# Kernel tuning notes

Hardware: AMD Instinct MI355X
Metric: run time of the kernel (lower is better)

The kernel has to match this reference:

```python
import jax, jax.numpy as jnp
import numpy as np

T = 1048576      # signal length
K = 3            # number of IMFs
ALPHA = 2000.0   # bandwidth penalty
TAU = 1e-7       # dual ascent step
TOL = 1e-6       # convergence tolerance
N_ITER = 50      # max fixed-point iterations


def _vmd(x, omega_init):
    T_ = x.shape[0]
    t = jnp.arange(1, T_ + 1, dtype=jnp.float32) / T_
    freqs = t - 0.5 - 1.0 / T_                           # [T]
    f_hat = jnp.fft.fftshift(jnp.fft.fft(x))             # [T] complex
    u0 = jnp.zeros((K, T_), dtype=f_hat.dtype)
    lam0 = jnp.zeros((T_,), dtype=f_hat.dtype)

    def step(carry, n):
        u_prev, lam_prev, omega, done = carry
        base = (freqs[None, :] - omega[:, None]) ** 2    # [K,T]
        # mode k's denom also gets (freqs-omega[k-1])^2 and (freqs-omega[k+1])^2
        nbr = jnp.zeros_like(base).at[1:].add(base[:-1]).at[:-1].add(base[1:])
        denom = base + nbr + TAU ** 2
        u_hat = (f_hat[None, :] - lam_prev[None, :] / 2.0) / (1.0 + ALPHA * denom)
        pw = jnp.real(u_hat) ** 2 + jnp.imag(u_hat) ** 2  # |u_hat|^2, [K,T]
        omega_new = jnp.sum(freqs[None, :] * pw, axis=1) / jnp.sum(pw, axis=1)
        lam_new = lam_prev + TAU * (jnp.sum(u_hat, axis=0) - f_hat)
        # convergence check (every 10th iter), mirrors the original break
        u_diff = jnp.sum(jnp.abs(u_hat - u_prev) ** 2) / jnp.sum(jnp.abs(u_prev) ** 2)
        om_diff = jnp.sum(jnp.abs(omega_new - jnp.roll(omega_new, 1))) / K
        conv = (n % 10 == 0) & (u_diff < TOL) & (om_diff < TOL)
        # freeze state once converged (break-iteration's fresh u_hat is kept)
        u_out = jnp.where(done, u_prev, u_hat)
        lam_out = jnp.where(done, lam_prev, lam_new)
        om_out = jnp.where(done, omega, omega_new)
        return (u_out, lam_out, om_out, done | conv), None

    init = (u0, lam0, omega_init.astype(jnp.float32), jnp.array(False))
    (u_hat, _, _, _), _ = jax.lax.scan(jax.checkpoint(step), init, jnp.arange(N_ITER))
    imfs = jnp.real(jnp.fft.ifft(jnp.fft.ifftshift(u_hat, axes=-1), axis=-1))
    return imfs.astype(jnp.float32)                      # [K,T]


def setup_inputs() -> dict:
    key = jax.random.key(0)
    kx, ko = jax.random.split(key)
    x = jax.random.normal(kx, (T,), dtype=jnp.float32)
    omega_init = jax.random.uniform(ko, (K,), dtype=jnp.float32) * 0.5  # init==1
    return {"x": x, "omega_init": omega_init}


def reference(x, omega_init):
    return _vmd(x, omega_init)
```

## Files before the change

kernel.cpp:

```cpp
#include <hip/hip_runtime.h>
#include <math.h>


#define ALPHA_F 2000.0f
#define TAU_F   1e-7f

static __device__ __forceinline__ int lpad2(int i) { return i + (i >> 4); }
static __device__ __forceinline__ int swz(int i)  { return ((i & 7) << 7) | (i >> 3); }
static __device__ __forceinline__ int swzA(int i) { return ((i & 7) << 6) | (i >> 3); }
static __device__ __forceinline__ float frcp(float x) { return __builtin_amdgcn_rcpf(x); }

typedef float v2f __attribute__((ext_vector_type(2)));
static __device__ __forceinline__ v2f sp(float s) { v2f r; r.x = s; r.y = s; return r; }
static __device__ __forceinline__ v2f v2(float a, float b) { v2f r; r.x = a; r.y = b; return r; }
static __device__ __forceinline__ v2f pkfma(v2f a, v2f b, v2f c)
{ return __builtin_elementwise_fma(a, b, c); }

#define PADN2 1088

template<int CTRL>
static __device__ __forceinline__ float dpp_addf(float v)
{
  int r = __builtin_amdgcn_update_dpp(0, __float_as_int(v), CTRL, 0xf, 0xf, true);
  return v + __int_as_float(r);
}
static __device__ __forceinline__ float wave64_sum(float v)
{
  v = dpp_addf<0x111>(v);
  v = dpp_addf<0x112>(v);
  v = dpp_addf<0x114>(v);
  v = dpp_addf<0x118>(v);
  v = dpp_addf<0x142>(v);
  v = dpp_addf<0x143>(v);
  return v;
}
static __device__ __forceinline__ float row16_sum(float v)
{
  v = dpp_addf<0x111>(v);
  v = dpp_addf<0x112>(v);
  v = dpp_addf<0x114>(v);
  v = dpp_addf<0x118>(v);
  return v;
}
static __device__ __forceinline__ float rdlane(float v, int l)
{
  return __int_as_float(__builtin_amdgcn_readlane(__float_as_int(v), l));
}

template<int SIGN>
static __device__ void fft1024c(float2* A, float2* B)
{
  const int u = threadIdx.x;
#pragma unroll
  for (int st = 0; st < 5; ++st) {
    float2 *in  = (st & 1) ? B : A;
    float2 *out = (st & 1) ? A : B;
    const int quarter = 1 << (2 * st);
    const int p = u & (quarter - 1);
    const int g = u >> (2 * st);

    float w1r, w1i;
    if (st == 0) { w1r = 1.0f; w1i = 0.0f; }
    else {
      float sw, cw;
      sincospif((float)(2 * p) * (1.0f / (float)(4 << (2 * st))), &sw, &cw);
      w1r = cw; w1i = (SIGN < 0) ? -sw : sw;
    }
    const float w2r = w1r*w1r - w1i*w1i,  w2i = 2.0f*w1r*w1i;
    const float w3r = w2r*w1r - w2i*w1i,  w3i = w2r*w1i + w2i*w1r;

    float2 X0 = in[lpad2(u      )];
    float2 X1 = in[lpad2(u + 256)];
    float2 X2 = in[lpad2(u + 512)];
    float2 X3 = in[lpad2(u + 768)];

    float y1r = X1.x*w1r - X1.y*w1i, y1i = X1.x*w1i + X1.y*w1r;
    float y2r = X2.x*w2r - X2.y*w2i, y2i = X2.x*w2i + X2.y*w2r;
    float y3r = X3.x*w3r - X3.y*w3i, y3i = X3.x*w3i + X3.y*w3r;

    float t0r = X0.x + y2r, t0i = X0.y + y2i;
    float t1r = X0.x - y2r, t1i = X0.y - y2i;
    float t2r = y1r + y3r,  t2i = y1i + y3i;
    float t3r = y1r - y3r,  t3i = y1i - y3i;

    float o0r = t0r + t2r, o0i = t0i + t2i;
    float o2r = t0r - t2r, o2i = t0i - t2i;
    float o1r, o1i, o3r, o3i;
    if (SIGN < 0) {
      o1r = t1r + t3i; o1i = t1i - t3r;
      o3r = t1r - t3i; o3i = t1i + t3r;
    } else {
      o1r = t1r - t3i; o1i = t1i + t3r;
      o3r = t1r + t3i; o3i = t1i - t3r;
    }
    const int base = (g << (2 * st + 2)) + p;
    out[lpad2(base              )] = make_float2(o0r, o0i);
    out[lpad2(base +     quarter)] = make_float2(o1r, o1i);
    out[lpad2(base + 2 * quarter)] = make_float2(o2r, o2i);
    out[lpad2(base + 3 * quarter)] = make_float2(o3r, o3i);
    __syncthreads();
  }
}

__global__ __launch_bounds__(256) void k_fwd_passA(const float* __restrict__ x,
                                                   float2* __restrict__ ws0)
{
  __shared__ float2 A[PADN2], B[PADN2];
  const int p = swzA(blockIdx.x);
  const int tid = threadIdx.x;
  const int c0 = 2 * p;
#pragma unroll
  for (int q = 0; q < 4; ++q) {
    int j = tid + 256 * q;
    A[lpad2(j)] = ((const float2*)x)[(size_t)j * 512 + p];
  }
  __syncthreads();
  fft1024c<-1>(A, B);
#pragma unroll
  for (int q = 0; q < 4; ++q) {
    int k = tid + 256 * q;
    int kk = (1024 - k) & 1023;
    float2 Z = B[lpad2(k)];
    float2 Wv = B[lpad2(kk)];
    float X0r = 0.5f * (Z.x + Wv.x), X0i = 0.5f * (Z.y - Wv.y);
    float X1r = 0.5f * (Z.y + Wv.y), X1i = 0.5f * (Wv.x - Z.x);
    int ph0 = c0 * k;
    int ph1 = ph0 + k;
    float s0, cc0, s1, cc1;
    sincospif((float)ph0 * (2.0f / 1048576.0f), &s0, &cc0);
    sincospif((float)ph1 * (2.0f / 1048576.0f), &s1, &cc1);
    float4 o;
    o.x = X0r * cc0 + X0i * s0; o.y = X0i * cc0 - X0r * s0;
    o.z = X1r * cc1 + X1i * s1; o.w = X1i * cc1 - X1r * s1;
    ((float4*)ws0)[(size_t)k * 512 + p] = o;
  }
}

__global__ __launch_bounds__(256) void k_fwd_passB(const float2* __restrict__ ws0,
                                                   float2* __restrict__ fhat,
                                                   float* __restrict__ ET)
{
  __shared__ float2 A[PADN2], B[PADN2];
  const int b = swz(blockIdx.x);
  const int tid = threadIdx.x;
#pragma unroll
  for (int q = 0; q < 4; ++q) {
    int j = tid + 256 * q;
    A[lpad2(j)] = ws0[(size_t)b * 1024 + j];
  }
  __syncthreads();
  fft1024c<-1>(A, B);
#pragma unroll
  for (int q = 0; q < 4; ++q) {
    int k2 = tid + 256 * q;
    float2 v = B[lpad2(k2)];
    fhat[(size_t)b * 1024 + k2] = v;
    ET[(size_t)k2 * 1024 + b] = v.x * v.x + v.y * v.y;
  }
}

static __device__ __forceinline__ void lag4(float x, float& l0, float& l1,
                                            float& l2, float& l3)
{
  float m0 = x, m1 = x - (1.0f / 3.0f), m2 = x - (2.0f / 3.0f), m3 = x - 1.0f;
  l0 = -4.5f * m1 * m2 * m3;
  l1 = 13.5f * m0 * m2 * m3;
  l2 = -13.5f * m0 * m1 * m3;
  l3 =  4.5f * m0 * m1 * m2;
}

__global__ __launch_bounds__(256) void k_moments(const float* __restrict__ ET,
                                                 double* __restrict__ W)
{
  __shared__ double red[4 * 4];
  const int B = blockIdx.x;
  const int k2 = B ^ 512;
  const int tid = threadIdx.x;
  double a0 = 0, a1 = 0, a2 = 0, a3 = 0;
#pragma unroll
  for (int q = 0; q < 4; ++q) {
    int k1 = tid + 256 * q;
    float e = ET[(size_t)k2 * 1024 + k1];
    float l0, l1, l2, l3;
    lag4((float)k1 * (1.0f / 1024.0f), l0, l1, l2, l3);
    a0 += (double)(e * l0); a1 += (double)(e * l1);
    a2 += (double)(e * l2); a3 += (double)(e * l3);
  }
  const int lane = tid & 63, wv = tid >> 6;
  double pv[4] = { a0, a1, a2, a3 };
#pragma unroll
  for (int j = 0; j < 4; ++j) {
    double v = pv[j];
    for (int off = 32; off; off >>= 1) v += __shfl_down(v, off, 64);
    if (lane == 0) red[wv * 4 + j] = v;
  }
  __syncthreads();
  if (tid < 4)
    W[B * 4 + tid] = red[tid] + red[4 + tid] + red[8 + tid] + red[12 + tid];
}

__global__ __launch_bounds__(1024) void k_solve(
    const double* __restrict__ W4, const float* __restrict__ omega_init,
    float* __restrict__ ckeepN, float* __restrict__ omegaF)
{
  __shared__ float red[2][6 * 16];
  const int t = threadIdx.x;
  const int lane = t & 63, wv = t >> 6;

  float Wsc[4], fsc[4];
#pragma unroll
  for (int e = 0; e < 4; ++e) {
    Wsc[e] = (float)W4[t * 4 + e];
    fsc[e] = (float)((double)t / 1024.0 + (double)e / 3072.0 - 0.5);
  }
  const v2f frP = v2(fsc[0], fsc[1]), frQ = v2(fsc[2], fsc[3]);
  const v2f WrP = v2(Wsc[0], Wsc[1]), WrQ = v2(Wsc[2], Wsc[3]);
  const v2f WfP = WrP * frP,          WfQ = WrQ * frQ;
  v2f cnrP = sp(0.0f), cnrQ = sp(0.0f);

  float om0 = omega_init[0], om1 = omega_init[1], om2 = omega_init[2];

#pragma unroll 1
  for (int it = 0; it < 49; ++it) {
    float* rb = red[it & 1];
    v2f p0 = sp(0.f), p1 = sp(0.f), p2 = sp(0.f),
        p3 = sp(0.f), p4 = sp(0.f), p5 = sp(0.f);

    auto node_pair = [&](const v2f fv, const v2f Wrv, const v2f Wfv, v2f& cnv) {
      v2f a0 = fv - sp(om0), a1 = fv - sp(om1), a2 = fv - sp(om2);
      v2f d0 = a0 * a0, d1 = a1 * a1, d2 = a2 * a2;
      v2f s01 = d0 + d1, s12 = d1 + d2;
      v2f dA = pkfma(sp(ALPHA_F), s01, sp(1.0f));
      v2f dC = pkfma(sp(ALPHA_F), s12, sp(1.0f));
      v2f dB = pkfma(sp(ALPHA_F), d2, dA);
      v2f AB = dA * dB, BC = dB * dC, AC = dA * dC;
      v2f ABC = AB * dC;
      v2f r = v2(frcp(ABC.x), frcp(ABC.y));
      v2f w0 = BC * r, w1 = AC * r, w2 = AB * r;
      v2f hf = pkfma(sp(-0.5f), cnv, sp(1.0f));
      v2f g = hf * hf;
      v2f gw0 = g * (w0 * w0), gw1 = g * (w1 * w1), gw2 = g * (w2 * w2);
      p0 = pkfma(Wfv, gw0, p0); p1 = pkfma(Wfv, gw1, p1); p2 = pkfma(Wfv, gw2, p2);
      p3 = pkfma(Wrv, gw0, p3); p4 = pkfma(Wrv, gw1, p4); p5 = pkfma(Wrv, gw2, p5);
      v2f S = (w0 + w1) + w2;
      cnv = pkfma(sp(TAU_F), pkfma(S, hf, sp(-1.0f)), cnv);
    };
    node_pair(frP, WrP, WfP, cnrP);
    node_pair(frQ, WrQ, WfQ, cnrQ);

    float q0 = p0.x + p0.y, q1 = p1.x + p1.y, q2 = p2.x + p2.y;
    float q3 = p3.x + p3.y, q4 = p4.x + p4.y, q5 = p5.x + p5.y;

    q0 = wave64_sum(q0); q1 = wave64_sum(q1); q2 = wave64_sum(q2);
    q3 = wave64_sum(q3); q4 = wave64_sum(q4); q5 = wave64_sum(q5);
    if (lane == 63) {
      rb[0 * 16 + wv] = q0; rb[1 * 16 + wv] = q1; rb[2 * 16 + wv] = q2;
      rb[3 * 16 + wv] = q3; rb[4 * 16 + wv] = q4; rb[5 * 16 + wv] = q5;
    }
    __syncthreads();
    float v1 = rb[lane];
    float v2_ = rb[64 + (lane & 31)];
    v1 = row16_sum(v1);
    v2_ = row16_sum(v2_);
    float n0 = rdlane(v1, 15), n1 = rdlane(v1, 31), n2 = rdlane(v1, 47);
    float e0 = rdlane(v1, 63), e1 = rdlane(v2_, 15), e2 = rdlane(v2_, 31);
    om0 = n0 * frcp(e0);
    om1 = n1 * frcp(e1);
    om2 = n2 * frcp(e2);
  }

  ((float4*)ckeepN)[t] = make_float4(cnrP.x, cnrP.y, cnrQ.x, cnrQ.y);
  if (t == 0) { omegaF[0] = om0; omegaF[1] = om1; omegaF[2] = om2; }
}

__global__ __launch_bounds__(256) void k_inv_A2(
    const float2* __restrict__ fhat, const float* __restrict__ ckeepN,
    const float* __restrict__ omegaF, float2* __restrict__ ws0)
{
  __shared__ float2 A[PADN2], B[PADN2];
  __shared__ float cn4[4096];
  __shared__ float som[3];
  const int tid = threadIdx.x;
  const int pk = blockIdx.x >> 10;
  const int b = swz(blockIdx.x & 1023);
  for (int i = tid; i < 4096; i += 256) cn4[i] = ckeepN[i];
  if (tid == 0) { som[0] = omegaF[0]; som[1] = omegaF[1]; som[2] = omegaF[2]; }
  __syncthreads();
  const float om0 = som[0], om1 = som[1], om2 = som[2];
  const float xb = (float)b * (1.0f / 1024.0f);
  float l0, l1, l2, l3, m0, m1, m2, m3;
  lag4(xb, l0, l1, l2, l3);
  lag4(1.0f - xb, m0, m1, m2, m3);

#pragma unroll
  for (int q = 0; q < 4; ++q) {
    int j = tid + 256 * q;
    float2 f = fhat[(size_t)b * 1024 + j];
    int bin = j ^ 512;
    int binp = 1023 - bin;
    float4 cv = ((const float4*)cn4)[bin];
    float4 cw = ((const float4*)cn4)[binp];
    float c  = l0 * cv.x + l1 * cv.y + l2 * cv.z + l3 * cv.w;
    float cp = m0 * cw.x + m1 * cw.y + m2 * cw.z + m3 * cw.w;
    float hf = 1.0f - 0.5f * c;
    float hp = 1.0f - 0.5f * cp;
    int tt = (bin << 10) | b;
    float freq = (float)tt * (1.0f / 1048576.0f) - 0.5f;
    float a0 = freq - om0, a1 = freq - om1, a2 = freq - om2;
    float d0 = a0 * a0, d1 = a1 * a1, d2 = a2 * a2;
    float g0 = -freq - om0, g1 = -freq - om1, g2 = -freq - om2;
    float e0 = g0 * g0, e1 = g1 * g1, e2 = g2 * g2;
    float2 V;
    if (pk == 0) {
      float r0  = hf * frcp(1.0f + ALPHA_F * (d0 + d1));
      float r0n = hp * frcp(1.0f + ALPHA_F * (e0 + e1));
      float r1  = hf * frcp(1.0f + ALPHA_F * (d0 + d1 + d2));
      float r1n = hp * frcp(1.0f + ALPHA_F * (e0 + e1 + e2));
      float Rr = 0.5f * (r0 + r0n);
      float Ri = 0.5f * (r1 + r1n);
      V = make_float2(f.x * Rr - f.y * Ri, f.x * Ri + f.y * Rr);
    } else {
      float r2  = hf * frcp(1.0f + ALPHA_F * (d1 + d2));
      float r2n = hp * frcp(1.0f + ALPHA_F * (e1 + e2));
      float Rr = 0.5f * (r2 + r2n);
      V = make_float2(f.x * Rr, f.y * Rr);
    }
    A[lpad2(j)] = V;
  }
  __syncthreads();
  fft1024c<1>(A, B);
#pragma unroll
  for (int q = 0; q < 4; ++q) {
    int m1i = tid + 256 * q;
    int ph = b * m1i;
    float s, c;
    sincospif((float)ph * (2.0f / 1048576.0f), &s, &c);
    float2 v = B[lpad2(m1i)];
    ws0[(size_t)pk * 1048576 + (size_t)m1i * 1024 + b]
        = make_float2(v.x * c - v.y * s, v.y * c + v.x * s);
  }
}

__global__ __launch_bounds__(256) void k_inv_B2(const float2* __restrict__ ws0,
                                                float* __restrict__ out)
{
  __shared__ float2 A[PADN2], B[PADN2];
  const int pk = blockIdx.x >> 10;
  const int b = swz(blockIdx.x & 1023);
  const int tid = threadIdx.x;
#pragma unroll
  for (int q = 0; q < 4; ++q) {
    int j = tid + 256 * q;
    A[lpad2(j)] = ws0[(size_t)pk * 1048576 + (size_t)b * 1024 + j];
  }
  __syncthreads();
  fft1024c<1>(A, B);
  const float sc = 1.0f / 1048576.0f;
#pragma unroll
  for (int q = 0; q < 4; ++q) {
    int m2 = tid + 256 * q;
    float2 v = B[lpad2(m2)];
    if (pk == 0) {
      out[(size_t)m2 * 1024 + b]           = v.x * sc;
      out[1048576 + (size_t)m2 * 1024 + b] = v.y * sc;
    } else {
      out[2097152 + (size_t)m2 * 1024 + b] = v.x * sc;
    }
  }
}

extern "C" void kernel_launch(void* const* d_in, const int* in_sizes, int n_in,
                              void* d_out, int out_size, void* d_ws, size_t ws_size,
                              hipStream_t stream)
{
  (void)in_sizes; (void)n_in; (void)out_size; (void)ws_size;
  const float* x       = (const float*)d_in[0];
  const float* om_init = (const float*)d_in[1];
  float* out = (float*)d_out;

  char* w = (char*)d_ws;
  const size_t MB = 1024ull * 1024ull;
  float2* fhat     = (float2*)(w);
  float*  ET       = (float*)(w + 8 * MB);
  double* W4       = (double*)(w + 12 * MB);
  float*  ckeepN   = (float*)(w + 12 * MB + 32 * 1024);
  float*  omegaF   = (float*)(w + 12 * MB + 48 * 1024);
  float2* scratch  = (float2*)(w + 16 * MB);

  k_fwd_passA<<<512, 256, 0, stream>>>(x, scratch);
  k_fwd_passB<<<1024, 256, 0, stream>>>(scratch, fhat, ET);
  k_moments<<<1024, 256, 0, stream>>>(ET, W4);
  k_solve<<<1, 1024, 0, stream>>>(W4, om_init, ckeepN, omegaF);
  k_inv_A2<<<2048, 256, 0, stream>>>(fhat, ckeepN, omegaF, scratch);
  k_inv_B2<<<2048, 256, 0, stream>>>(scratch, out);
}
```

Before: 184.0 us.

## Precompute FFT twiddle table, recur post-FFT twiddles, and use packed float2 math

Adds a small kernel that builds radix-4 twiddle tables for both FFT directions once; each FFT block stages the table into LDS instead of calling sincospi per stage. The first radix-4 stage is specialised to drop its trivial twiddles. The inter-pass twiddles in the forward and inverse first passes now come from a complex recurrence instead of two sincospi calls per element. Butterflies and the Wiener filter use packed v2f math. The trade-offs are an extra kernel launch, more LDS per block (which may lower occupancy), and some accuracy loss from the recurrence.

Result: slower. 190.1 us (+3.3%).

```diff
diff --git a/kernel.cpp b/kernel.cpp
--- a/kernel.cpp
+++ b/kernel.cpp
@@ -15,6 +15,12 @@
 static __device__ __forceinline__ v2f v2(float a, float b) { v2f r; r.x = a; r.y = b; return r; }
 static __device__ __forceinline__ v2f pkfma(v2f a, v2f b, v2f c)
 { return __builtin_elementwise_fma(a, b, c); }
+static __device__ __forceinline__ v2f cmul(v2f a, v2f w)
+{
+  v2f t = a * sp(w.x);
+  v2f s = v2(-a.y, a.x);
+  return pkfma(s, sp(w.y), t);
+}
 
 #define PADN2 1088
 
@@ -47,114 +53,148 @@
   return __int_as_float(__builtin_amdgcn_readlane(__float_as_int(v), l));
 }
 
+__global__ __launch_bounds__(256) void k_twid(float2* __restrict__ tw)
+{
+  int i = threadIdx.x + blockIdx.x * 256;
+  if (i >= 340) return;
+  int st, p;
+  if (i < 4)       { st = 1; p = i; }
+  else if (i < 20) { st = 2; p = i - 4; }
+  else if (i < 84) { st = 3; p = i - 20; }
+  else             { st = 4; p = i - 84; }
+  float sw, cw;
+  sincospif((float)(2 * p) * (1.0f / (float)(4 << (2 * st))), &sw, &cw);
+#pragma unroll
+  for (int dir = 0; dir < 2; ++dir) {
+    float w1r = cw, w1i = dir ? sw : -sw;
+    float w2r = w1r * w1r - w1i * w1i, w2i = 2.0f * w1r * w1i;
+    float w3r = w2r * w1r - w2i * w1i, w3i = w2r * w1i + w2i * w1r;
+    float2* b = tw + dir * 1020;
+    b[i]       = make_float2(w1r, w1i);
+    b[340 + i] = make_float2(w2r, w2i);
+    b[680 + i] = make_float2(w3r, w3i);
+  }
+}
+
 template<int SIGN>
-static __device__ void fft1024c(float2* A, float2* B)
+static __device__ void fft1024p(v2f* A, v2f* B, const v2f* __restrict__ twl)
 {
   const int u = threadIdx.x;
-#pragma unroll
-  for (int st = 0; st < 5; ++st) {
-    float2 *in  = (st & 1) ? B : A;
-    float2 *out = (st & 1) ? A : B;
+  {
+    v2f X0 = A[lpad2(u)], X1 = A[lpad2(u + 256)];
+    v2f X2 = A[lpad2(u + 512)], X3 = A[lpad2(u + 768)];
+    v2f t0 = X0 + X2, t1 = X0 - X2, t2 = X1 + X3, t3 = X1 - X3;
+    v2f o0 = t0 + t2, o2 = t0 - t2;
+    v2f s3 = t3.yx;
+    v2f ns3 = v2(s3.x, -s3.y);
+    v2f o1, o3;
+    if (SIGN < 0) { o1 = t1 + ns3; o3 = t1 - ns3; }
+    else          { o1 = t1 - ns3; o3 = t1 + ns3; }
+    const int base = u << 2;
+    B[lpad2(base    )] = o0; B[lpad2(base + 1)] = o1;
+    B[lpad2(base + 2)] = o2; B[lpad2(base + 3)] = o3;
+    __syncthreads();
+  }
+#pragma unroll
+  for (int st = 1; st < 5; ++st) {
+    v2f *in  = (st & 1) ? B : A;
+    v2f *out = (st & 1) ? A : B;
     const int quarter = 1 << (2 * st);
     const int p = u & (quarter - 1);
     const int g = u >> (2 * st);
-
-    float w1r, w1i;
-    if (st == 0) { w1r = 1.0f; w1i = 0.0f; }
-    else {
-      float sw, cw;
-      sincospif((float)(2 * p) * (1.0f / (float)(4 << (2 * st))), &sw, &cw);
-      w1r = cw; w1i = (SIGN < 0) ? -sw : sw;
-    }
-    const float w2r = w1r*w1r - w1i*w1i,  w2i = 2.0f*w1r*w1i;
-    const float w3r = w2r*w1r - w2i*w1i,  w3i = w2r*w1i + w2i*w1r;
-
-    float2 X0 = in[lpad2(u      )];
-    float2 X1 = in[lpad2(u + 256)];
-    float2 X2 = in[lpad2(u + 512)];
-    float2 X3 = in[lpad2(u + 768)];
-
-    float y1r = X1.x*w1r - X1.y*w1i, y1i = X1.x*w1i + X1.y*w1r;
-    float y2r = X2.x*w2r - X2.y*w2i, y2i = X2.x*w2i + X2.y*w2r;
-    float y3r = X3.x*w3r - X3.y*w3i, y3i = X3.x*w3i + X3.y*w3r;
-
-    float t0r = X0.x + y2r, t0i = X0.y + y2i;
-    float t1r = X0.x - y2r, t1i = X0.y - y2i;
-    float t2r = y1r + y3r,  t2i = y1i + y3i;
-    float t3r = y1r - y3r,  t3i = y1i - y3i;
-
-    float o0r = t0r + t2r, o0i = t0i + t2i;
-    float o2r = t0r - t2r, o2i = t0i - t2i;
-    float o1r, o1i, o3r, o3i;
-    if (SIGN < 0) {
-      o1r = t1r + t3i; o1i = t1i - t3r;
-      o3r = t1r - t3i; o3i = t1i + t3r;
-    } else {
-      o1r = t1r - t3i; o1i = t1i + t3r;
-      o3r = t1r + t3i; o3i = t1i - t3r;
-    }
+    const int ti = (quarter - 4) / 3 + p;
+
+    v2f w1 = twl[ti], w2 = twl[340 + ti], w3 = twl[680 + ti];
+
+    v2f X0 = in[lpad2(u)], X1 = in[lpad2(u + 256)];
+    v2f X2 = in[lpad2(u + 512)], X3 = in[lpad2(u + 768)];
+
+    v2f y1 = cmul(X1, w1), y2 = cmul(X2, w2), y3 = cmul(X3, w3);
+
+    v2f t0 = X0 + y2, t1 = X0 - y2, t2 = y1 + y3, t3 = y1 - y3;
+    v2f o0 = t0 + t2, o2 = t0 - t2;
+    v2f s3 = t3.yx;
+    v2f ns3 = v2(s3.x, -s3.y);
+    v2f o1, o3;
+    if (SIGN < 0) { o1 = t1 + ns3; o3 = t1 - ns3; }
+    else          { o1 = t1 - ns3; o3 = t1 + ns3; }
+
     const int base = (g << (2 * st + 2)) + p;
-    out[lpad2(base              )] = make_float2(o0r, o0i);
-    out[lpad2(base +     quarter)] = make_float2(o1r, o1i);
-    out[lpad2(base + 2 * quarter)] = make_float2(o2r, o2i);
-    out[lpad2(base + 3 * quarter)] = make_float2(o3r, o3i);
+    out[lpad2(base              )] = o0;
+    out[lpad2(base +     quarter)] = o1;
+    out[lpad2(base + 2 * quarter)] = o2;
+    out[lpad2(base + 3 * quarter)] = o3;
     __syncthreads();
   }
 }
 
+#define STAGE_TW(dst, src) \
+  for (int i_ = threadIdx.x; i_ < 510; i_ += 256) \
+    ((float4*)(dst))[i_] = ((const float4*)(src))[i_];
+
 __global__ __launch_bounds__(256) void k_fwd_passA(const float* __restrict__ x,
+                                                   const float2* __restrict__ twg,
                                                    float2* __restrict__ ws0)
 {
-  __shared__ float2 A[PADN2], B[PADN2];
+  __shared__ __align__(16) v2f A[PADN2], B[PADN2];
+  __shared__ __align__(16) v2f twl[1020];
   const int p = swzA(blockIdx.x);
   const int tid = threadIdx.x;
   const int c0 = 2 * p;
+  STAGE_TW(twl, twg);
 #pragma unroll
   for (int q = 0; q < 4; ++q) {
     int j = tid + 256 * q;
-    A[lpad2(j)] = ((const float2*)x)[(size_t)j * 512 + p];
-  }
-  __syncthreads();
-  fft1024c<-1>(A, B);
+    A[lpad2(j)] = ((const v2f*)x)[(size_t)j * 512 + p];
+  }
+  __syncthreads();
+  fft1024p<-1>(A, B, twl);
+
+  float sa, ca, sb, cb, ssa, cca, ssb, ccb;
+  sincospif((float)(c0 * tid) * (2.0f / 1048576.0f), &sa, &ca);
+  sincospif((float)((c0 + 1) * tid) * (2.0f / 1048576.0f), &sb, &cb);
+  sincospif((float)c0 * (1.0f / 2048.0f), &ssa, &cca);
+  sincospif((float)(c0 + 1) * (1.0f / 2048.0f), &ssb, &ccb);
+  v2f E0 = v2(ca, -sa), E1 = v2(cb, -sb);
+  const v2f S0 = v2(cca, -ssa), S1 = v2(ccb, -ssb);
 #pragma unroll
   for (int q = 0; q < 4; ++q) {
     int k = tid + 256 * q;
     int kk = (1024 - k) & 1023;
-    float2 Z = B[lpad2(k)];
-    float2 Wv = B[lpad2(kk)];
+    v2f Z = B[lpad2(k)];
+    v2f Wv = B[lpad2(kk)];
     float X0r = 0.5f * (Z.x + Wv.x), X0i = 0.5f * (Z.y - Wv.y);
     float X1r = 0.5f * (Z.y + Wv.y), X1i = 0.5f * (Wv.x - Z.x);
-    int ph0 = c0 * k;
-    int ph1 = ph0 + k;
-    float s0, cc0, s1, cc1;
-    sincospif((float)ph0 * (2.0f / 1048576.0f), &s0, &cc0);
-    sincospif((float)ph1 * (2.0f / 1048576.0f), &s1, &cc1);
-    float4 o;
-    o.x = X0r * cc0 + X0i * s0; o.y = X0i * cc0 - X0r * s0;
-    o.z = X1r * cc1 + X1i * s1; o.w = X1i * cc1 - X1r * s1;
+    v2f o01 = cmul(v2(X0r, X0i), E0);
+    v2f o23 = cmul(v2(X1r, X1i), E1);
+    float4 o = make_float4(o01.x, o01.y, o23.x, o23.y);
     ((float4*)ws0)[(size_t)k * 512 + p] = o;
+    E0 = cmul(E0, S0); E1 = cmul(E1, S1);
   }
 }
 
 __global__ __launch_bounds__(256) void k_fwd_passB(const float2* __restrict__ ws0,
+                                                   const float2* __restrict__ twg,
                                                    float2* __restrict__ fhat,
                                                    float* __restrict__ ET)
 {
-  __shared__ float2 A[PADN2], B[PADN2];
+  __shared__ __align__(16) v2f A[PADN2], B[PADN2];
+  __shared__ __align__(16) v2f twl[1020];
   const int b = swz(blockIdx.x);
   const int tid = threadIdx.x;
+  STAGE_TW(twl, twg);
 #pragma unroll
   for (int q = 0; q < 4; ++q) {
     int j = tid + 256 * q;
-    A[lpad2(j)] = ws0[(size_t)b * 1024 + j];
-  }
-  __syncthreads();
-  fft1024c<-1>(A, B);
+    A[lpad2(j)] = ((const v2f*)ws0)[(size_t)b * 1024 + j];
+  }
+  __syncthreads();
+  fft1024p<-1>(A, B, twl);
 #pragma unroll
   for (int q = 0; q < 4; ++q) {
     int k2 = tid + 256 * q;
-    float2 v = B[lpad2(k2)];
-    fhat[(size_t)b * 1024 + k2] = v;
+    v2f v = B[lpad2(k2)];
+    fhat[(size_t)b * 1024 + k2] = make_float2(v.x, v.y);
     ET[(size_t)k2 * 1024 + b] = v.x * v.x + v.y * v.y;
   }
 }
@@ -275,14 +315,17 @@
 
 __global__ __launch_bounds__(256) void k_inv_A2(
     const float2* __restrict__ fhat, const float* __restrict__ ckeepN,
-    const float* __restrict__ omegaF, float2* __restrict__ ws0)
-{
-  __shared__ float2 A[PADN2], B[PADN2];
+    const float* __restrict__ omegaF, const float2* __restrict__ twg,
+    float2* __restrict__ ws0)
+{
+  __shared__ __align__(16) v2f A[PADN2], B[PADN2];
+  __shared__ __align__(16) v2f twl[1020];
   __shared__ float cn4[4096];
   __shared__ float som[3];
   const int tid = threadIdx.x;
   const int pk = blockIdx.x >> 10;
   const int b = swz(blockIdx.x & 1023);
+  STAGE_TW(twl, twg);
   for (int i = tid; i < 4096; i += 256) cn4[i] = ckeepN[i];
   if (tid == 0) { som[0] = omegaF[0]; som[1] = omegaF[1]; som[2] = omegaF[2]; }
   __syncthreads();
@@ -306,60 +349,65 @@
     float hp = 1.0f - 0.5f * cp;
     int tt = (bin << 10) | b;
     float freq = (float)tt * (1.0f / 1048576.0f) - 0.5f;
-    float a0 = freq - om0, a1 = freq - om1, a2 = freq - om2;
-    float d0 = a0 * a0, d1 = a1 * a1, d2 = a2 * a2;
-    float g0 = -freq - om0, g1 = -freq - om1, g2 = -freq - om2;
-    float e0 = g0 * g0, e1 = g1 * g1, e2 = g2 * g2;
-    float2 V;
+    v2f fpm = v2(freq, -freq);
+    v2f A0 = fpm - sp(om0), A1 = fpm - sp(om1), A2v = fpm - sp(om2);
+    v2f D0 = A0 * A0, D1 = A1 * A1, D2 = A2v * A2v;
+    v2f V;
     if (pk == 0) {
-      float r0  = hf * frcp(1.0f + ALPHA_F * (d0 + d1));
-      float r0n = hp * frcp(1.0f + ALPHA_F * (e0 + e1));
-      float r1  = hf * frcp(1.0f + ALPHA_F * (d0 + d1 + d2));
-      float r1n = hp * frcp(1.0f + ALPHA_F * (e0 + e1 + e2));
-      float Rr = 0.5f * (r0 + r0n);
-      float Ri = 0.5f * (r1 + r1n);
-      V = make_float2(f.x * Rr - f.y * Ri, f.x * Ri + f.y * Rr);
+      v2f DA = pkfma(sp(ALPHA_F), D0 + D1, sp(1.0f));
+      v2f DB = pkfma(sp(ALPHA_F), D2, DA);
+      float r0 = hf * frcp(DA.x), r0n = hp * frcp(DA.y);
+      float r1 = hf * frcp(DB.x), r1n = hp * frcp(DB.y);
+      float Rr = 0.5f * (r0 + r0n), Ri = 0.5f * (r1 + r1n);
+      V = cmul(v2(f.x, f.y), v2(Rr, Ri));
     } else {
-      float r2  = hf * frcp(1.0f + ALPHA_F * (d1 + d2));
-      float r2n = hp * frcp(1.0f + ALPHA_F * (e1 + e2));
+      v2f DC = pkfma(sp(ALPHA_F), D1 + D2, sp(1.0f));
+      float r2 = hf * frcp(DC.x), r2n = hp * frcp(DC.y);
       float Rr = 0.5f * (r2 + r2n);
-      V = make_float2(f.x * Rr, f.y * Rr);
+      V = v2(f.x, f.y) * sp(Rr);
     }
     A[lpad2(j)] = V;
   }
   __syncthreads();
-  fft1024c<1>(A, B);
+  fft1024p<1>(A, B, twl);
+
+  float sa, ca, ss, cs;
+  sincospif((float)(b * tid) * (2.0f / 1048576.0f), &sa, &ca);
+  sincospif((float)b * (1.0f / 2048.0f), &ss, &cs);
+  v2f E = v2(ca, sa);
+  const v2f S = v2(cs, ss);
 #pragma unroll
   for (int q = 0; q < 4; ++q) {
     int m1i = tid + 256 * q;
-    int ph = b * m1i;
-    float s, c;
-    sincospif((float)ph * (2.0f / 1048576.0f), &s, &c);
-    float2 v = B[lpad2(m1i)];
-    ws0[(size_t)pk * 1048576 + (size_t)m1i * 1024 + b]
-        = make_float2(v.x * c - v.y * s, v.y * c + v.x * s);
+    v2f v = B[lpad2(m1i)];
+    v2f o = cmul(v, E);
+    ws0[(size_t)pk * 1048576 + (size_t)m1i * 1024 + b] = make_float2(o.x, o.y);
+    E = cmul(E, S);
   }
 }
 
 __global__ __launch_bounds__(256) void k_inv_B2(const float2* __restrict__ ws0,
+                                                const float2* __restrict__ twg,
                                                 float* __restrict__ out)
 {
-  __shared__ float2 A[PADN2], B[PADN2];
+  __shared__ __align__(16) v2f A[PADN2], B[PADN2];
+  __shared__ __align__(16) v2f twl[1020];
   const int pk = blockIdx.x >> 10;
   const int b = swz(blockIdx.x & 1023);
   const int tid = threadIdx.x;
+  STAGE_TW(twl, twg);
 #pragma unroll
   for (int q = 0; q < 4; ++q) {
     int j = tid + 256 * q;
-    A[lpad2(j)] = ws0[(size_t)pk * 1048576 + (size_t)b * 1024 + j];
-  }
-  __syncthreads();
-  fft1024c<1>(A, B);
+    A[lpad2(j)] = ((const v2f*)ws0)[(size_t)pk * 1048576 + (size_t)b * 1024 + j];
+  }
+  __syncthreads();
+  fft1024p<1>(A, B, twl);
   const float sc = 1.0f / 1048576.0f;
 #pragma unroll
   for (int q = 0; q < 4; ++q) {
     int m2 = tid + 256 * q;
-    float2 v = B[lpad2(m2)];
+    v2f v = B[lpad2(m2)];
     if (pk == 0) {
       out[(size_t)m2 * 1024 + b]           = v.x * sc;
       out[1048576 + (size_t)m2 * 1024 + b] = v.y * sc;
@@ -385,12 +433,14 @@
   double* W4       = (double*)(w + 12 * MB);
   float*  ckeepN   = (float*)(w + 12 * MB + 32 * 1024);
   float*  omegaF   = (float*)(w + 12 * MB + 48 * 1024);
+  float2* tw       = (float2*)(w + 12 * MB + 64 * 1024);
   float2* scratch  = (float2*)(w + 16 * MB);
 
-  k_fwd_passA<<<512, 256, 0, stream>>>(x, scratch);
-  k_fwd_passB<<<1024, 256, 0, stream>>>(scratch, fhat, ET);
+  k_twid<<<2, 256, 0, stream>>>(tw);
+  k_fwd_passA<<<512, 256, 0, stream>>>(x, tw, scratch);
+  k_fwd_passB<<<1024, 256, 0, stream>>>(scratch, tw, fhat, ET);
   k_moments<<<1024, 256, 0, stream>>>(ET, W4);
   k_solve<<<1, 1024, 0, stream>>>(W4, om_init, ckeepN, omegaF);
-  k_inv_A2<<<2048, 256, 0, stream>>>(fhat, ckeepN, omegaF, scratch);
-  k_inv_B2<<<2048, 256, 0, stream>>>(scratch, out);
-}
+  k_inv_A2<<<2048, 256, 0, stream>>>(fhat, ckeepN, omegaF, tw + 1020, scratch);
+  k_inv_B2<<<2048, 256, 0, stream>>>(scratch, tw + 1020, out);
+}
```
